# Optimization experiments

Measured on AMD Instinct MI355X. Metric: run time of the kernel, lower is better.

## Reference

```python
import jax, jax.numpy as jnp
import numpy as np

N = 50000   # nodes
E = 800000  # edges (avg degree 16)
F = 64      # n_feat
P = 20      # pos_enc (RWPE dim)
H = 64      # n_hidden
G = 500     # graphs in batch (100 nodes each)


def setup_inputs() -> dict:
    key = jax.random.key(0)
    ks = jax.random.split(key, 32)
    w = lambda k, s: jax.random.normal(k, s, jnp.float32) * 0.05
    inp = {
        "x": jax.random.normal(ks[0], (N, F), jnp.float32),
        "RWPE": jax.random.normal(ks[1], (N, P), jnp.float32),
        "W_rw": w(ks[2], (P, F)), "b_rw": jnp.zeros((F,), jnp.float32),
    }
    for i in range(5):
        din = F if i == 0 else H
        inp[f"Wc{i+1}"] = w(ks[3 + i], (din, H))
        inp[f"bc{i+1}"] = jnp.zeros((H,), jnp.float32)
        inp[f"Wp{i+1}"] = w(ks[8 + i], (din, H))
        inp[f"bp{i+1}"] = jnp.zeros((H,), jnp.float32)
    inp["gamma"] = jnp.ones((H,), jnp.float32)
    inp["beta"] = jnp.zeros((H,), jnp.float32)
    inp["edge_index"] = jax.random.randint(ks[14], (2, E), 0, N, jnp.int32)
    inp["ptr"] = (jnp.arange(G + 1, dtype=jnp.int32) * (N // G))
    return inp


def _gcn_conv(h, W, b, src, dst, dinv):
    # GCNConv: symmetric-normalized aggregation with self-loops, then bias.
    h = h @ W                                             # [N, H]
    msg = h[src] * (dinv[src] * dinv[dst])[:, None]       # [E, H]
    agg = jax.ops.segment_sum(msg, dst, num_segments=N)
    agg = agg + h * (dinv * dinv)[:, None]                # self-loop term
    return agg + b


def reference(x, RWPE, W_rw, b_rw,
              Wc1, bc1, Wc2, bc2, Wc3, bc3, Wc4, bc4, Wc5, bc5,
              Wp1, bp1, Wp2, bp2, Wp3, bp3, Wp4, bp4, Wp5, bp5,
              gamma, beta, edge_index, ptr):
    src, dst = edge_index[0], edge_index[1]
    deg = jax.ops.segment_sum(jnp.ones((E,), jnp.float32), dst, num_segments=N) + 1.0
    dinv = jax.lax.rsqrt(deg)

    pe = RWPE @ W_rw + b_rw                               # Linear_RW
    h = x + pe
    h = jax.nn.relu(_gcn_conv(h, Wc1, bc1, src, dst, dinv))
    # memory_error branch: LapPE = zeros -> no-op add
    convs = [(Wc2, bc2), (Wc3, bc3), (Wc4, bc4), (Wc5, bc5)]
    conps = [(Wp1, bp1), (Wp2, bp2), (Wp3, bp3), (Wp4, bp4)]
    for (Wc, bc), (Wp, bp) in zip(convs, conps):
        pe = jax.nn.relu(_gcn_conv(pe, Wp, bp, src, dst, dinv))
        h = h + pe
        h = _gcn_conv(h, Wc, bc, src, dst, dinv)
        if (Wc is not Wc5):
            h = jax.nn.relu(h)
    # conv5 output goes through BatchNorm1d (training stats) then relu
    mu = jnp.mean(h, axis=0)
    var = jnp.var(h, axis=0)
    h = (h - mu) * jax.lax.rsqrt(var + 1e-5) * gamma + beta
    h = jax.nn.relu(h)
    # segment_csr mean pooling over ptr
    counts = ptr[1:] - ptr[:-1]
    seg = jnp.repeat(jnp.arange(G, dtype=jnp.int32), counts, total_repeat_length=N)
    pooled = jax.ops.segment_sum(h, seg, num_segments=G)
    return pooled / counts[:, None].astype(h.dtype)
```

## Files before the change

kernel.cpp:

```cpp
#include <hip/hip_runtime.h>
#include <hip/hip_fp16.h>

#define NN 50000
#define NE 800000
#define FD 64
#define PD 20
#define NG 500
#define NXCD 8
#define DRANGE 6250
#define CHUNK_E 2048


__global__ void k_deg_xcd(const int* __restrict__ dstA, int* __restrict__ deg) {
    int xcd = blockIdx.x & 7;
    int chunk = blockIdx.x >> 3;
    int lo = xcd * DRANGE;
    int hi = lo + DRANGE;
    int base = chunk * CHUNK_E;
    int end = min(base + CHUNK_E, NE);
    for (int i = base + threadIdx.x; i < end; i += 256) {
        int d = dstA[i];
        if (d >= lo && d < hi) atomicAdd(&deg[d], 1);
    }
}

__global__ void k_scan1(const int* __restrict__ deg, int* __restrict__ rowp,
                        int* __restrict__ bsum, float* __restrict__ dinv) {
    __shared__ int lds[256];
    int t = threadIdx.x;
    int idx = blockIdx.x * 256 + t;
    int v = (idx < NN) ? deg[idx] : 0;
    if (idx < NN) dinv[idx] = rsqrtf((float)v + 1.0f);
    lds[t] = v;
    __syncthreads();
    for (int off = 1; off < 256; off <<= 1) {
        int add = (t >= off) ? lds[t - off] : 0;
        __syncthreads();
        lds[t] += add;
        __syncthreads();
    }
    if (idx < NN) rowp[idx + 1] = lds[t];
    if (t == 255) bsum[blockIdx.x] = lds[255];
}

__global__ void k_scan2(int* bsum, int nB) {
    __shared__ int lds[256];
    int t = threadIdx.x;
    lds[t] = (t < nB) ? bsum[t] : 0;
    __syncthreads();
    for (int off = 1; off < 256; off <<= 1) {
        int add = (t >= off) ? lds[t - off] : 0;
        __syncthreads();
        lds[t] += add;
        __syncthreads();
    }
    if (t < nB) bsum[t] = lds[t];
}

__global__ void k_scan3(int* __restrict__ rowp, const int* __restrict__ bsum,
                        int* __restrict__ fill) {
    int idx = blockIdx.x * 256 + threadIdx.x;
    if (idx == 0) { rowp[0] = 0; fill[0] = 0; }
    if (idx < NN) {
        int v = rowp[idx + 1];
        if (blockIdx.x > 0) { v += bsum[blockIdx.x - 1]; rowp[idx + 1] = v; }
        if (idx + 1 < NN) fill[idx + 1] = v;
    }
}

__global__ void k_csr_fill_xcd(const int* __restrict__ srcA, const int* __restrict__ dstA,
                               const float* __restrict__ dinv,
                               int* __restrict__ fill, int2* __restrict__ meta) {
    int xcd = blockIdx.x & 7;
    int chunk = blockIdx.x >> 3;
    int lo = xcd * DRANGE;
    int hi = lo + DRANGE;
    int base = chunk * CHUNK_E;
    int end = min(base + CHUNK_E, NE);
    for (int i = base + threadIdx.x; i < end; i += 256) {
        int d = dstA[i];
        if (d >= lo && d < hi) {
            int s = srcA[i];
            int pos = atomicAdd(&fill[d], 1);
            int2 m;
            m.x = s;
            m.y = __float_as_int(dinv[s]);
            meta[pos] = m;
        }
    }
}


__global__ void k_pe(const float* __restrict__ x, const float* __restrict__ rwpe,
                     const float* __restrict__ Wrw, const float* __restrict__ brw,
                     __half* __restrict__ outI) {
    __shared__ float Wl[PD * FD];
    __shared__ float rows[4 * PD];
    int t = threadIdx.x;
    int nodeBase = blockIdx.x * 4;
    for (int i = t; i < PD * FD; i += 256) Wl[i] = Wrw[i];
    if (t < 4 * PD) {
        int n = nodeBase + t / PD;
        rows[t] = (n < NN) ? rwpe[n * PD + (t % PD)] : 0.f;
    }
    __syncthreads();
    int f = t & 63, sl = t >> 6;
    int node = nodeBase + sl;
    if (node < NN) {
        float acc = brw[f];
        #pragma unroll
        for (int k = 0; k < PD; k++) acc += rows[sl * PD + k] * Wl[k * FD + f];
        outI[(size_t)node * 128 + f]      = __float2half_rn(x[node * FD + f] + acc);
        outI[(size_t)node * 128 + 64 + f] = __float2half_rn(acc);
    }
}

__device__ inline void acc8(float* acc, uint4 v, float w) {
    const __half2* h = reinterpret_cast<const __half2*>(&v);
    float2 f0 = __half22float2(h[0]);
    float2 f1 = __half22float2(h[1]);
    float2 f2 = __half22float2(h[2]);
    float2 f3 = __half22float2(h[3]);
    acc[0] += w * f0.x; acc[1] += w * f0.y;
    acc[2] += w * f1.x; acc[3] += w * f1.y;
    acc[4] += w * f2.x; acc[5] += w * f2.y;
    acc[6] += w * f3.x; acc[7] += w * f3.y;
}

__device__ inline void acc4(float* acc, uint2 v, float w) {
    const __half2* h = reinterpret_cast<const __half2*>(&v);
    float2 f0 = __half22float2(h[0]);
    float2 f1 = __half22float2(h[1]);
    acc[0] += w * f0.x; acc[1] += w * f0.y;
    acc[2] += w * f1.x; acc[3] += w * f1.y;
}

template <bool FINAL>
__global__ __launch_bounds__(256) void k_dual(
    const __half* __restrict__ in,
    const float* __restrict__ dinv, const int* __restrict__ rowp,
    const int2* __restrict__ meta,
    const float* __restrict__ Wc, const float* __restrict__ bc,
    const float* __restrict__ Wp, const float* __restrict__ bp,
    __half* __restrict__ out, int write_pe,
    float* __restrict__ foutF)
{
    __shared__ float Wl[64 * 64];
    __shared__ float aggH[16 * 68];
    __shared__ float aggP[16 * 68];
    int t = threadIdx.x;

    {
        const float4* W4 = reinterpret_cast<const float4*>(Wc);
        float4* Wl4 = reinterpret_cast<float4*>(Wl);
        #pragma unroll
        for (int i = 0; i < 4; i++) Wl4[t + 256 * i] = W4[t + 256 * i];
    }

    int l = t & 15;
    int sl = t >> 4;
    int ws = (t >> 4) & 3;
    int node = blockIdx.x * 16 + sl;
    int e0 = rowp[node], e1 = rowp[node + 1];
    int cnt = e1 - e0;
    float dd = dinv[node];

    if (!FINAL) {
        const uint4* base = reinterpret_cast<const uint4*>(in);
        float acc[8] = {0, 0, 0, 0, 0, 0, 0, 0};
        for (int cb = 0; cb < cnt; cb += 16) {
            int midx = min(e0 + cb + l, NE - 1);
            int2 mreg = meta[midx];
            int rem = cnt - cb;
            int src0 = __shfl(mreg.x, ws * 16, 64);
            #pragma unroll
            for (int g = 0; g < 2; g++) {
                if (g == 1 && rem <= 8) break;
                int srcj[8]; float wj[8];
                #pragma unroll
                for (int jj = 0; jj < 8; jj++) {
                    int j = g * 8 + jj;
                    int sx = __shfl(mreg.x, ws * 16 + j, 64);
                    float ww = __int_as_float(__shfl(mreg.y, ws * 16 + j, 64));
                    bool valid = (j < rem);
                    srcj[jj] = valid ? sx : src0;
                    wj[jj] = valid ? ww : 0.f;
                }
                uint4 v0 = base[(size_t)srcj[0] * 16 + l];
                uint4 v1 = base[(size_t)srcj[1] * 16 + l];
                uint4 v2 = base[(size_t)srcj[2] * 16 + l];
                uint4 v3 = base[(size_t)srcj[3] * 16 + l];
                uint4 v4 = base[(size_t)srcj[4] * 16 + l];
                uint4 v5 = base[(size_t)srcj[5] * 16 + l];
                uint4 v6 = base[(size_t)srcj[6] * 16 + l];
                uint4 v7 = base[(size_t)srcj[7] * 16 + l];
                acc8(acc, v0, wj[0]);
                acc8(acc, v1, wj[1]);
                acc8(acc, v2, wj[2]);
                acc8(acc, v3, wj[3]);
                acc8(acc, v4, wj[4]);
                acc8(acc, v5, wj[5]);
                acc8(acc, v6, wj[6]);
                acc8(acc, v7, wj[7]);
            }
        }
        float s[8];
        {
            uint4 sv = base[(size_t)node * 16 + l];
            const __half2* h = reinterpret_cast<const __half2*>(&sv);
            float2 f0 = __half22float2(h[0]);
            float2 f1 = __half22float2(h[1]);
            float2 f2 = __half22float2(h[2]);
            float2 f3 = __half22float2(h[3]);
            s[0] = f0.x; s[1] = f0.y; s[2] = f1.x; s[3] = f1.y;
            s[4] = f2.x; s[5] = f2.y; s[6] = f3.x; s[7] = f3.y;
        }
        float* dst = (l < 8) ? &aggH[sl * 68 + l * 8] : &aggP[sl * 68 + (l - 8) * 8];
        float4* d4 = reinterpret_cast<float4*>(dst);
        d4[0] = make_float4(dd * acc[0] + dd * dd * s[0],
                            dd * acc[1] + dd * dd * s[1],
                            dd * acc[2] + dd * dd * s[2],
                            dd * acc[3] + dd * dd * s[3]);
        d4[1] = make_float4(dd * acc[4] + dd * dd * s[4],
                            dd * acc[5] + dd * dd * s[5],
                            dd * acc[6] + dd * dd * s[6],
                            dd * acc[7] + dd * dd * s[7]);
    } else {
        const uint2* base2 = reinterpret_cast<const uint2*>(in);
        float acc[4] = {0, 0, 0, 0};
        for (int cb = 0; cb < cnt; cb += 16) {
            int midx = min(e0 + cb + l, NE - 1);
            int2 mreg = meta[midx];
            int rem = cnt - cb;
            int src0 = __shfl(mreg.x, ws * 16, 64);
            #pragma unroll
            for (int g = 0; g < 2; g++) {
                if (g == 1 && rem <= 8) break;
                int srcj[8]; float wj[8];
                #pragma unroll
                for (int jj = 0; jj < 8; jj++) {
                    int j = g * 8 + jj;
                    int sx = __shfl(mreg.x, ws * 16 + j, 64);
                    float ww = __int_as_float(__shfl(mreg.y, ws * 16 + j, 64));
                    bool valid = (j < rem);
                    srcj[jj] = valid ? sx : src0;
                    wj[jj] = valid ? ww : 0.f;
                }
                uint2 v0 = base2[(size_t)srcj[0] * 32 + l];
                uint2 v1 = base2[(size_t)srcj[1] * 32 + l];
                uint2 v2 = base2[(size_t)srcj[2] * 32 + l];
                uint2 v3 = base2[(size_t)srcj[3] * 32 + l];
                uint2 v4 = base2[(size_t)srcj[4] * 32 + l];
                uint2 v5 = base2[(size_t)srcj[5] * 32 + l];
                uint2 v6 = base2[(size_t)srcj[6] * 32 + l];
                uint2 v7 = base2[(size_t)srcj[7] * 32 + l];
                acc4(acc, v0, wj[0]);
                acc4(acc, v1, wj[1]);
                acc4(acc, v2, wj[2]);
                acc4(acc, v3, wj[3]);
                acc4(acc, v4, wj[4]);
                acc4(acc, v5, wj[5]);
                acc4(acc, v6, wj[6]);
                acc4(acc, v7, wj[7]);
            }
        }
        float s[4];
        {
            uint2 sv = base2[(size_t)node * 32 + l];
            const __half2* h = reinterpret_cast<const __half2*>(&sv);
            float2 f0 = __half22float2(h[0]);
            float2 f1 = __half22float2(h[1]);
            s[0] = f0.x; s[1] = f0.y; s[2] = f1.x; s[3] = f1.y;
        }
        float4* d4 = reinterpret_cast<float4*>(&aggH[sl * 68 + l * 4]);
        d4[0] = make_float4(dd * acc[0] + dd * dd * s[0],
                            dd * acc[1] + dd * dd * s[1],
                            dd * acc[2] + dd * dd * s[2],
                            dd * acc[3] + dd * dd * s[3]);
    }
    __syncthreads();

    int c = t & 15;
    int sl2 = t >> 4;
    int onode = blockIdx.x * 16 + sl2;
    float4 oh = *reinterpret_cast<const float4*>(bc + c * 4);
    {
        const float* arow = &aggH[sl2 * 68];
        #pragma unroll 16
        for (int k = 0; k < 64; k++) {
            float av = arow[k];
            float4 wv = *reinterpret_cast<const float4*>(&Wl[k * 64 + c * 4]);
            oh.x += av * wv.x; oh.y += av * wv.y; oh.z += av * wv.z; oh.w += av * wv.w;
        }
    }
    if (FINAL) {
        *reinterpret_cast<float4*>(foutF + (size_t)onode * 64 + c * 4) = oh;
        return;
    }
    oh.x = fmaxf(oh.x, 0.f); oh.y = fmaxf(oh.y, 0.f);
    oh.z = fmaxf(oh.z, 0.f); oh.w = fmaxf(oh.w, 0.f);

    __syncthreads();
    {
        const float4* W4 = reinterpret_cast<const float4*>(Wp);
        float4* Wl4 = reinterpret_cast<float4*>(Wl);
        #pragma unroll
        for (int i = 0; i < 4; i++) Wl4[t + 256 * i] = W4[t + 256 * i];
    }
    __syncthreads();

    float4 op = *reinterpret_cast<const float4*>(bp + c * 4);
    {
        const float* arow = &aggP[sl2 * 68];
        #pragma unroll 16
        for (int k = 0; k < 64; k++) {
            float av = arow[k];
            float4 wv = *reinterpret_cast<const float4*>(&Wl[k * 64 + c * 4]);
            op.x += av * wv.x; op.y += av * wv.y; op.z += av * wv.z; op.w += av * wv.w;
        }
    }
    op.x = fmaxf(op.x, 0.f); op.y = fmaxf(op.y, 0.f);
    op.z = fmaxf(op.z, 0.f); op.w = fmaxf(op.w, 0.f);

    uint2* out2 = reinterpret_cast<uint2*>(out);
    {
        __half2 a = __floats2half2_rn(oh.x + op.x, oh.y + op.y);
        __half2 b = __floats2half2_rn(oh.z + op.z, oh.w + op.w);
        uint2 u;
        u.x = *reinterpret_cast<unsigned int*>(&a);
        u.y = *reinterpret_cast<unsigned int*>(&b);
        out2[(size_t)onode * 32 + c] = u;
    }
    if (write_pe) {
        __half2 a = __floats2half2_rn(op.x, op.y);
        __half2 b = __floats2half2_rn(op.z, op.w);
        uint2 u;
        u.x = *reinterpret_cast<unsigned int*>(&a);
        u.y = *reinterpret_cast<unsigned int*>(&b);
        out2[(size_t)onode * 32 + 16 + c] = u;
    }
}


__global__ void k_bnstats(const float* __restrict__ h, float* __restrict__ stats) {
    __shared__ float s1[256], s2[256];
    int t = threadIdx.x;
    int f = t & 63, sl = t >> 6;
    float a = 0.f, b = 0.f;
    for (int node = blockIdx.x * 4 + sl; node < NN; node += gridDim.x * 4) {
        float v = h[node * 64 + f];
        a += v;
        b += v * v;
    }
    s1[t] = a;
    s2[t] = b;
    __syncthreads();
    if (t < 64) {
        a = s1[t] + s1[t + 64] + s1[t + 128] + s1[t + 192];
        b = s2[t] + s2[t + 64] + s2[t + 128] + s2[t + 192];
        atomicAdd(&stats[t], a);
        atomicAdd(&stats[64 + t], b);
    }
}

__global__ void k_bnfinal(float* stats) {
    int f = threadIdx.x;
    if (f < 64) {
        float mu = stats[f] / (float)NN;
        float var = stats[64 + f] / (float)NN - mu * mu;
        stats[f] = mu;
        stats[64 + f] = rsqrtf(var + 1e-5f);
    }
}

__global__ void k_pool(const float* __restrict__ h, const float* __restrict__ stats,
                       const float* __restrict__ gamma, const float* __restrict__ beta,
                       const int* __restrict__ ptr, float* __restrict__ out) {
    int g = blockIdx.x;
    int f = threadIdx.x;
    int s = ptr[g], e = ptr[g + 1];
    float mu = stats[f], rstd = stats[64 + f], ga = gamma[f], be = beta[f];
    float acc = 0.f;
    for (int n = s; n < e; n++) {
        float v = (h[n * 64 + f] - mu) * rstd * ga + be;
        acc += fmaxf(v, 0.f);
    }
    out[g * 64 + f] = acc / (float)(e - s);
}


extern "C" void kernel_launch(void* const* d_in, const int* in_sizes, int n_in,
                              void* d_out, int out_size, void* d_ws, size_t ws_size,
                              hipStream_t stream) {
    const float* x    = (const float*)d_in[0];
    const float* rwpe = (const float*)d_in[1];
    const float* Wrw  = (const float*)d_in[2];
    const float* brw  = (const float*)d_in[3];
    const float *Wc[5], *bc[5], *Wp[5], *bp[5];
    for (int i = 0; i < 5; i++) {
        Wc[i] = (const float*)d_in[4 + 4 * i];
        bc[i] = (const float*)d_in[5 + 4 * i];
        Wp[i] = (const float*)d_in[6 + 4 * i];
        bp[i] = (const float*)d_in[7 + 4 * i];
    }
    const float* gamma = (const float*)d_in[24];
    const float* beta  = (const float*)d_in[25];
    const int* ei  = (const int*)d_in[26];
    const int* ptr = (const int*)d_in[27];
    float* out = (float*)d_out;

    char* wsp = (char*)d_ws;
    auto alloc = [&](size_t bytes) { void* p = (void*)wsp; wsp += ((bytes + 255) / 256) * 256; return p; };
    int*    deg   = (int*)alloc(NN * 4);
    int*    rowp  = (int*)alloc((NN + 1) * 4);
    int*    fill  = (int*)alloc(NN * 4);
    int2*   meta  = (int2*)alloc((size_t)NE * 8);
    float*  dinv  = (float*)alloc(NN * 4);
    __half* bufP  = (__half*)alloc((size_t)NN * 128 * 2);
    __half* bufQ  = (__half*)alloc((size_t)NN * 128 * 2);
    float*  bufF  = (float*)alloc((size_t)NN * 64 * 4);
    float*  stats = (float*)alloc(512);
    int*    bsum  = (int*)alloc(256 * 4);

    hipMemsetAsync(deg, 0, NN * 4, stream);
    hipMemsetAsync(stats, 0, 512, stream);

    const int* srcA = ei;
    const int* dstA = ei + NE;

    dim3 b256(256);
    int gN = (NN + 255) / 256;
    int gNode16 = NN / 16;
    int gFill = ((NE + CHUNK_E - 1) / CHUNK_E) * 8;

    k_deg_xcd<<<gFill, b256, 0, stream>>>(dstA, deg);
    k_scan1<<<gN, b256, 0, stream>>>(deg, rowp, bsum, dinv);
    k_scan2<<<1, b256, 0, stream>>>(bsum, gN);
    k_scan3<<<gN, b256, 0, stream>>>(rowp, bsum, fill);
    k_csr_fill_xcd<<<gFill, b256, 0, stream>>>(srcA, dstA, dinv, fill, meta);

    k_pe<<<(NN + 3) / 4, b256, 0, stream>>>(x, rwpe, Wrw, brw, bufP);

    k_dual<false><<<gNode16, b256, 0, stream>>>(
        bufP, dinv, rowp, meta, Wc[0], bc[0], Wp[0], bp[0], bufQ, 1, nullptr);
    k_dual<false><<<gNode16, b256, 0, stream>>>(
        bufQ, dinv, rowp, meta, Wc[1], bc[1], Wp[1], bp[1], bufP, 1, nullptr);
    k_dual<false><<<gNode16, b256, 0, stream>>>(
        bufP, dinv, rowp, meta, Wc[2], bc[2], Wp[2], bp[2], bufQ, 1, nullptr);
    k_dual<false><<<gNode16, b256, 0, stream>>>(
        bufQ, dinv, rowp, meta, Wc[3], bc[3], Wp[3], bp[3], bufP, 0, nullptr);
    k_dual<true><<<gNode16, b256, 0, stream>>>(
        bufP, dinv, rowp, meta, Wc[4], bc[4], nullptr, nullptr, nullptr, 0, bufF);

    k_bnstats<<<256, b256, 0, stream>>>(bufF, stats);
    k_bnfinal<<<1, 64, 0, stream>>>(stats);
    k_pool<<<NG, 64, 0, stream>>>(bufF, stats, gamma, beta, ptr, out);
}
```

Measured before the change: 340.5 us.

## Double threads per node in fused GCN layer kernel, split edges across halves

The fused dual-GCN kernel now launches 512 threads per block. Each node gets 32 lanes, and two half-groups take interleaved edges, then combine their partial sums with a cross-lane shuffle. Both weight matrices are loaded into shared memory up front, and the two 64x64 transforms run at the same time on separate halves of the block instead of one after the other with a reload. This aims to expose more memory-level parallelism in the gather and remove a serialized weight reload, at the cost of more shared memory, an extra barrier, and a shuffle reduction.

```diff
diff --git a/kernel.cpp b/kernel.cpp
--- a/kernel.cpp
+++ b/kernel.cpp
@@ -136,7 +136,7 @@
 }
 
 template <bool FINAL>
-__global__ __launch_bounds__(256) void k_dual(
+__global__ __launch_bounds__(512) void k_dual(
     const __half* __restrict__ in,
     const float* __restrict__ dinv, const int* __restrict__ rowp,
     const int2* __restrict__ meta,
@@ -145,21 +145,30 @@
     __half* __restrict__ out, int write_pe,
     float* __restrict__ foutF)
 {
-    __shared__ float Wl[64 * 64];
+    __shared__ float WcL[64 * 64];
+    __shared__ float WpL[FINAL ? 4 : 64 * 64];
     __shared__ float aggH[16 * 68];
-    __shared__ float aggP[16 * 68];
+    __shared__ float aggP[FINAL ? 4 : 16 * 68];
     int t = threadIdx.x;
 
     {
         const float4* W4 = reinterpret_cast<const float4*>(Wc);
-        float4* Wl4 = reinterpret_cast<float4*>(Wl);
-        #pragma unroll
-        for (int i = 0; i < 4; i++) Wl4[t + 256 * i] = W4[t + 256 * i];
-    }
-
-    int l = t & 15;
-    int sl = t >> 4;
-    int ws = (t >> 4) & 3;
+        float4* WL4 = reinterpret_cast<float4*>(WcL);
+        WL4[t] = W4[t];
+        WL4[t + 512] = W4[t + 512];
+        if (!FINAL) {
+            const float4* P4 = reinterpret_cast<const float4*>(Wp);
+            float4* PL4 = reinterpret_cast<float4*>(WpL);
+            PL4[t] = P4[t];
+            PL4[t + 512] = P4[t + 512];
+        }
+    }
+
+    int sl = t >> 5;
+    int l32 = t & 31;
+    int half = l32 >> 4;
+    int l = l32 & 15;
+    int baseLane = (sl & 1) * 32;
     int node = blockIdx.x * 16 + sl;
     int e0 = rowp[node], e1 = rowp[node + 1];
     int cnt = e1 - e0;
@@ -167,24 +176,25 @@
 
     if (!FINAL) {
         const uint4* base = reinterpret_cast<const uint4*>(in);
+        uint4 sv = base[(size_t)node * 16 + l];
         float acc[8] = {0, 0, 0, 0, 0, 0, 0, 0};
-        for (int cb = 0; cb < cnt; cb += 16) {
-            int midx = min(e0 + cb + l, NE - 1);
+        for (int cb = 0; cb < cnt; cb += 32) {
+            int midx = min(e0 + cb + l32, e1 - 1);
             int2 mreg = meta[midx];
             int rem = cnt - cb;
-            int src0 = __shfl(mreg.x, ws * 16, 64);
+            int src0 = __shfl(mreg.x, baseLane, 64);
             #pragma unroll
             for (int g = 0; g < 2; g++) {
-                if (g == 1 && rem <= 8) break;
+                if (g == 1 && rem <= 16) break;
                 int srcj[8]; float wj[8];
                 #pragma unroll
-                for (int jj = 0; jj < 8; jj++) {
-                    int j = g * 8 + jj;
-                    int sx = __shfl(mreg.x, ws * 16 + j, 64);
-                    float ww = __int_as_float(__shfl(mreg.y, ws * 16 + j, 64));
+                for (int kk = 0; kk < 8; kk++) {
+                    int j = 2 * (g * 8 + kk) + half;
+                    int sx = __shfl(mreg.x, baseLane + j, 64);
+                    float ww = __int_as_float(__shfl(mreg.y, baseLane + j, 64));
                     bool valid = (j < rem);
-                    srcj[jj] = valid ? sx : src0;
-                    wj[jj] = valid ? ww : 0.f;
+                    srcj[kk] = valid ? sx : src0;
+                    wj[kk] = valid ? ww : 0.f;
                 }
                 uint4 v0 = base[(size_t)srcj[0] * 16 + l];
                 uint4 v1 = base[(size_t)srcj[1] * 16 + l];
@@ -204,47 +214,47 @@
                 acc8(acc, v7, wj[7]);
             }
         }
-        float s[8];
-        {
-            uint4 sv = base[(size_t)node * 16 + l];
+        #pragma unroll
+        for (int i = 0; i < 8; i++) acc[i] += __shfl_xor(acc[i], 16, 64);
+        if (half == 0) {
             const __half2* h = reinterpret_cast<const __half2*>(&sv);
             float2 f0 = __half22float2(h[0]);
             float2 f1 = __half22float2(h[1]);
             float2 f2 = __half22float2(h[2]);
             float2 f3 = __half22float2(h[3]);
-            s[0] = f0.x; s[1] = f0.y; s[2] = f1.x; s[3] = f1.y;
-            s[4] = f2.x; s[5] = f2.y; s[6] = f3.x; s[7] = f3.y;
-        }
-        float* dst = (l < 8) ? &aggH[sl * 68 + l * 8] : &aggP[sl * 68 + (l - 8) * 8];
-        float4* d4 = reinterpret_cast<float4*>(dst);
-        d4[0] = make_float4(dd * acc[0] + dd * dd * s[0],
-                            dd * acc[1] + dd * dd * s[1],
-                            dd * acc[2] + dd * dd * s[2],
-                            dd * acc[3] + dd * dd * s[3]);
-        d4[1] = make_float4(dd * acc[4] + dd * dd * s[4],
-                            dd * acc[5] + dd * dd * s[5],
-                            dd * acc[6] + dd * dd * s[6],
-                            dd * acc[7] + dd * dd * s[7]);
+            float s[8] = {f0.x, f0.y, f1.x, f1.y, f2.x, f2.y, f3.x, f3.y};
+            float* dst = (l < 8) ? &aggH[sl * 68 + l * 8] : &aggP[sl * 68 + (l - 8) * 8];
+            float4* d4 = reinterpret_cast<float4*>(dst);
+            d4[0] = make_float4(dd * acc[0] + dd * dd * s[0],
+                                dd * acc[1] + dd * dd * s[1],
+                                dd * acc[2] + dd * dd * s[2],
+                                dd * acc[3] + dd * dd * s[3]);
+            d4[1] = make_float4(dd * acc[4] + dd * dd * s[4],
+                                dd * acc[5] + dd * dd * s[5],
+                                dd * acc[6] + dd * dd * s[6],
+                                dd * acc[7] + dd * dd * s[7]);
+        }
     } else {
         const uint2* base2 = reinterpret_cast<const uint2*>(in);
+        uint2 sv = base2[(size_t)node * 32 + l];
         float acc[4] = {0, 0, 0, 0};
-        for (int cb = 0; cb < cnt; cb += 16) {
-            int midx = min(e0 + cb + l, NE - 1);
+        for (int cb = 0; cb < cnt; cb += 32) {
+            int midx = min(e0 + cb + l32, e1 - 1);
             int2 mreg = meta[midx];
             int rem = cnt - cb;
-            int src0 = __shfl(mreg.x, ws * 16, 64);
+            int src0 = __shfl(mreg.x, baseLane, 64);
             #pragma unroll
             for (int g = 0; g < 2; g++) {
-                if (g == 1 && rem <= 8) break;
+                if (g == 1 && rem <= 16) break;
                 int srcj[8]; float wj[8];
                 #pragma unroll
-                for (int jj = 0; jj < 8; jj++) {
-                    int j = g * 8 + jj;
-                    int sx = __shfl(mreg.x, ws * 16 + j, 64);
-                    float ww = __int_as_float(__shfl(mreg.y, ws * 16 + j, 64));
+                for (int kk = 0; kk < 8; kk++) {
+                    int j = 2 * (g * 8 + kk) + half;
+                    int sx = __shfl(mreg.x, baseLane + j, 64);
+                    float ww = __int_as_float(__shfl(mreg.y, baseLane + j, 64));
                     bool valid = (j < rem);
-                    srcj[jj] = valid ? sx : src0;
-                    wj[jj] = valid ? ww : 0.f;
+                    srcj[kk] = valid ? sx : src0;
+                    wj[kk] = valid ? ww : 0.f;
                 }
                 uint2 v0 = base2[(size_t)srcj[0] * 32 + l];
                 uint2 v1 = base2[(size_t)srcj[1] * 32 + l];
@@ -264,80 +274,77 @@
                 acc4(acc, v7, wj[7]);
             }
         }
-        float s[4];
-        {
-            uint2 sv = base2[(size_t)node * 32 + l];
+        #pragma unroll
+        for (int i = 0; i < 4; i++) acc[i] += __shfl_xor(acc[i], 16, 64);
+        if (half == 0) {
             const __half2* h = reinterpret_cast<const __half2*>(&sv);
             float2 f0 = __half22float2(h[0]);
             float2 f1 = __half22float2(h[1]);
-            s[0] = f0.x; s[1] = f0.y; s[2] = f1.x; s[3] = f1.y;
-        }
-        float4* d4 = reinterpret_cast<float4*>(&aggH[sl * 68 + l * 4]);
-        d4[0] = make_float4(dd * acc[0] + dd * dd * s[0],
-                            dd * acc[1] + dd * dd * s[1],
-                            dd * acc[2] + dd * dd * s[2],
-                            dd * acc[3] + dd * dd * s[3]);
+            float s[4] = {f0.x, f0.y, f1.x, f1.y};
+            float4* d4 = reinterpret_cast<float4*>(&aggH[sl * 68 + l * 4]);
+            d4[0] = make_float4(dd * acc[0] + dd * dd * s[0],
+                                dd * acc[1] + dd * dd * s[1],
+                                dd * acc[2] + dd * dd * s[2],
+                                dd * acc[3] + dd * dd * s[3]);
+        }
     }
     __syncthreads();
 
     int c = t & 15;
-    int sl2 = t >> 4;
+    int sl2 = (t >> 4) & 15;
     int onode = blockIdx.x * 16 + sl2;
-    float4 oh = *reinterpret_cast<const float4*>(bc + c * 4);
-    {
+    float4 oh = make_float4(0.f, 0.f, 0.f, 0.f);
+    float4 op = make_float4(0.f, 0.f, 0.f, 0.f);
+    if (t < 256) {
+        oh = *reinterpret_cast<const float4*>(bc + c * 4);
         const float* arow = &aggH[sl2 * 68];
         #pragma unroll 16
         for (int k = 0; k < 64; k++) {
             float av = arow[k];
-            float4 wv = *reinterpret_cast<const float4*>(&Wl[k * 64 + c * 4]);
+            float4 wv = *reinterpret_cast<const float4*>(&WcL[k * 64 + c * 4]);
             oh.x += av * wv.x; oh.y += av * wv.y; oh.z += av * wv.z; oh.w += av * wv.w;
         }
-    }
-    if (FINAL) {
-        *reinterpret_cast<float4*>(foutF + (size_t)onode * 64 + c * 4) = oh;
-        return;
-    }
-    oh.x = fmaxf(oh.x, 0.f); oh.y = fmaxf(oh.y, 0.f);
-    oh.z = fmaxf(oh.z, 0.f); oh.w = fmaxf(oh.w, 0.f);
-
-    __syncthreads();
-    {
-        const float4* W4 = reinterpret_cast<const float4*>(Wp);
-        float4* Wl4 = reinterpret_cast<float4*>(Wl);
-        #pragma unroll
-        for (int i = 0; i < 4; i++) Wl4[t + 256 * i] = W4[t + 256 * i];
-    }
-    __syncthreads();
-
-    float4 op = *reinterpret_cast<const float4*>(bp + c * 4);
-    {
+        if (FINAL) {
+            *reinterpret_cast<float4*>(foutF + (size_t)onode * 64 + c * 4) = oh;
+        }
+    } else if (!FINAL) {
+        op = *reinterpret_cast<const float4*>(bp + c * 4);
         const float* arow = &aggP[sl2 * 68];
         #pragma unroll 16
         for (int k = 0; k < 64; k++) {
             float av = arow[k];
-            float4 wv = *reinterpret_cast<const float4*>(&Wl[k * 64 + c * 4]);
+            float4 wv = *reinterpret_cast<const float4*>(&WpL[k * 64 + c * 4]);
             op.x += av * wv.x; op.y += av * wv.y; op.z += av * wv.z; op.w += av * wv.w;
         }
-    }
-    op.x = fmaxf(op.x, 0.f); op.y = fmaxf(op.y, 0.f);
-    op.z = fmaxf(op.z, 0.f); op.w = fmaxf(op.w, 0.f);
-
+        op.x = fmaxf(op.x, 0.f); op.y = fmaxf(op.y, 0.f);
+        op.z = fmaxf(op.z, 0.f); op.w = fmaxf(op.w, 0.f);
+    }
+    if (FINAL) return;
+
+    __syncthreads();
     uint2* out2 = reinterpret_cast<uint2*>(out);
-    {
-        __half2 a = __floats2half2_rn(oh.x + op.x, oh.y + op.y);
-        __half2 b = __floats2half2_rn(oh.z + op.z, oh.w + op.w);
+    if (t >= 256) {
+        *reinterpret_cast<float4*>(&aggH[sl2 * 68 + c * 4]) = op;
+        if (write_pe) {
+            __half2 a = __floats2half2_rn(op.x, op.y);
+            __half2 b = __floats2half2_rn(op.z, op.w);
+            uint2 u;
+            u.x = *reinterpret_cast<unsigned int*>(&a);
+            u.y = *reinterpret_cast<unsigned int*>(&b);
+            out2[(size_t)onode * 32 + 16 + c] = u;
+        }
+    }
+    __syncthreads();
+    if (t < 256) {
+        oh.x = fmaxf(oh.x, 0.f); oh.y = fmaxf(oh.y, 0.f);
+        oh.z = fmaxf(oh.z, 0.f); oh.w = fmaxf(oh.w, 0.f);
+        float4 opv = *reinterpret_cast<const float4*>(&aggH[sl2 * 68 + c * 4]);
+        __half2 a = __floats2half2_rn(oh.x + opv.x, oh.y + opv.y);
+        __half2 b = __floats2half2_rn(oh.z + opv.z, oh.w + opv.w);
         uint2 u;
         u.x = *reinterpret_cast<unsigned int*>(&a);
         u.y = *reinterpret_cast<unsigned int*>(&b);
         out2[(size_t)onode * 32 + c] = u;
-    }
-    if (write_pe) {
-        __half2 a = __floats2half2_rn(op.x, op.y);
-        __half2 b = __floats2half2_rn(op.z, op.w);
-        uint2 u;
-        u.x = *reinterpret_cast<unsigned int*>(&a);
-        u.y = *reinterpret_cast<unsigned int*>(&b);
-        out2[(size_t)onode * 32 + 16 + c] = u;
     }
 }
 
@@ -429,6 +436,7 @@
     const int* dstA = ei + NE;
 
     dim3 b256(256);
+    dim3 b512(512);
     int gN = (NN + 255) / 256;
     int gNode16 = NN / 16;
     int gFill = ((NE + CHUNK_E - 1) / CHUNK_E) * 8;
@@ -441,15 +449,15 @@
 
     k_pe<<<(NN + 3) / 4, b256, 0, stream>>>(x, rwpe, Wrw, brw, bufP);
 
-    k_dual<false><<<gNode16, b256, 0, stream>>>(
+    k_dual<false><<<gNode16, b512, 0, stream>>>(
         bufP, dinv, rowp, meta, Wc[0], bc[0], Wp[0], bp[0], bufQ, 1, nullptr);
-    k_dual<false><<<gNode16, b256, 0, stream>>>(
+    k_dual<false><<<gNode16, b512, 0, stream>>>(
         bufQ, dinv, rowp, meta, Wc[1], bc[1], Wp[1], bp[1], bufP, 1, nullptr);
-    k_dual<false><<<gNode16, b256, 0, stream>>>(
+    k_dual<false><<<gNode16, b512, 0, stream>>>(
         bufP, dinv, rowp, meta, Wc[2], bc[2], Wp[2], bp[2], bufQ, 1, nullptr);
-    k_dual<false><<<gNode16, b256, 0, stream>>>(
+    k_dual<false><<<gNode16, b512, 0, stream>>>(
         bufQ, dinv, rowp, meta, Wc[3], bc[3], Wp[3], bp[3], bufP, 0, nullptr);
-    k_dual<true><<<gNode16, b256, 0, stream>>>(
+    k_dual<true><<<gNode16, b512, 0, stream>>>(
         bufP, dinv, rowp, meta, Wc[4], bc[4], nullptr, nullptr, nullptr, 0, bufF);
 
     k_bnstats<<<256, b256, 0, stream>>>(bufF, stats);
```

Measured after the change: 450.3 us. +32.2%, slower.
